# Kernel optimization log

Hardware: AMD Instinct MI355X
Metric: run time of the kernel (lower is better)

Reference implementation:

```python
import jax, jax.numpy as jnp
import numpy as np

D_IN = 30


def setup_inputs() -> dict:
    key = jax.random.key(0)
    ks = jax.random.split(key, 12)
    N, E = 100000, 3200000
    h = jax.random.normal(ks[0], (N, D_IN), dtype=jnp.float32)
    edge_index = jax.random.randint(ks[1], (2, E), 0, N, dtype=jnp.int64)
    edge_weight = jax.random.uniform(ks[2], (E,), dtype=jnp.float32)
    s = 1.0 / np.sqrt(D_IN)
    convW = jax.random.uniform(ks[3], (D_IN, D_IN), jnp.float32, -s, s)
    convb = jax.random.uniform(ks[4], (D_IN,), jnp.float32, -s, s)
    w1 = jax.random.uniform(ks[5], (30, 10), jnp.float32, -s, s)
    b1 = jax.random.uniform(ks[6], (10,), jnp.float32, -s, s)
    s2 = 1.0 / np.sqrt(10)
    w2 = jax.random.uniform(ks[7], (10, 10), jnp.float32, -s2, s2)
    b2 = jax.random.uniform(ks[8], (10,), jnp.float32, -s2, s2)
    w3 = jax.random.uniform(ks[9], (10, 10), jnp.float32, -s2, s2)
    b3 = jax.random.uniform(ks[10], (10,), jnp.float32, -s2, s2)
    w4 = jax.random.uniform(ks[11], (10, 1), jnp.float32, -s2, s2)
    b4 = jnp.zeros((1,), jnp.float32)
    return {"h": h, "edge_index": edge_index, "edge_weight": edge_weight,
            "convW": convW, "convb": convb,
            "w1": w1, "b1": b1, "w2": w2, "b2": b2,
            "w3": w3, "b3": b3, "w4": w4, "b4": b4}


def gcn_conv(h, edge_index, edge_weight, W, b):
    N = h.shape[0]
    x = h @ W  # [N, 30] linear transform first (PyG GCNConv)
    loop = jnp.arange(N, dtype=edge_index.dtype)
    row = jnp.concatenate([edge_index[0], loop])  # sources
    col = jnp.concatenate([edge_index[1], loop])  # targets
    ew = jnp.concatenate([edge_weight, jnp.ones((N,), edge_weight.dtype)])
    deg = jax.ops.segment_sum(ew, col, num_segments=N)
    dis = jnp.where(deg > 0, jax.lax.rsqrt(deg), 0.0)
    norm = dis[row] * ew * dis[col]  # symmetric normalization
    msg = x[row] * norm[:, None]  # [E+N, 30] gather + scale
    out = jax.ops.segment_sum(msg, col, num_segments=N)  # scatter-add
    return out + b


def reference(h, edge_index, edge_weight, convW, convb,
              w1, b1, w2, b2, w3, b3, w4, b4):
    x = jax.nn.relu(gcn_conv(h, edge_index, edge_weight, convW, convb))
    x = jax.nn.relu(x @ w1 + b1)
    x = jax.nn.relu(x @ w2 + b2)
    x = jax.nn.relu(x @ w3 + b3)
    x = jax.nn.sigmoid(x @ w4 + b4)
    return x[:, 0]
```

## Files before the change

kernel.cpp:

```cpp
#include <hip/hip_runtime.h>
#include <hip/hip_fp16.h>
#include <math.h>

#define D 30
#define FIXS 16777216.0f
#define FIXA 1048576.0f
#define BKT 128
#define LGB 7
#define CHUNK 8192
#define CAP 4608
#define ROWBITS 18
#define ROWMASK ((1u << ROWBITS) - 1)
#define MAXBKT 1024

__global__ __launch_bounds__(1024) void scatter1p_kernel(const int* __restrict__ row,
                                                         const int* __restrict__ col,
                                                         const float* __restrict__ ew,
                                                         unsigned* __restrict__ ecnt,
                                                         uint2* __restrict__ keysw,
                                                         int E, int nbkt) {
    __shared__ unsigned gcur[MAXBKT];
    __shared__ unsigned lofs[MAXBKT];
    __shared__ unsigned lcnt[MAXBKT];
    __shared__ unsigned sscan[1024];
    __shared__ uint2 st[CHUNK];
    __shared__ unsigned short bkt[CHUNK];
    const int t = threadIdx.x;
    for (int i = t; i < nbkt; i += 1024) lcnt[i] = 0;
    __syncthreads();

    const int e0 = blockIdx.x * CHUNK;
    const int e1 = min(e0 + CHUNK, E);
    const int cc = e1 - e0;
    const int nv = cc >> 2;
    const int4* c4 = (const int4*)(col + e0);

    for (int i = t; i < nv; i += 1024) {
        const int4 c = c4[i];
        atomicAdd(&lcnt[c.x >> LGB], 1u);
        atomicAdd(&lcnt[c.y >> LGB], 1u);
        atomicAdd(&lcnt[c.z >> LGB], 1u);
        atomicAdd(&lcnt[c.w >> LGB], 1u);
    }
    for (int e = e0 + (nv << 2) + t; e < e1; e += 1024) atomicAdd(&lcnt[col[e] >> LGB], 1u);
    __syncthreads();

    {
        const unsigned v = (t < nbkt) ? lcnt[t] : 0u;
        sscan[t] = v;
        for (int off = 1; off < 1024; off <<= 1) {
            __syncthreads();
            const unsigned x = (t >= off) ? sscan[t - off] : 0u;
            __syncthreads();
            sscan[t] += x;
        }
        __syncthreads();
        if (t < nbkt) {
            lofs[t] = sscan[t] - v;
            gcur[t] = (v > 0) ? atomicAdd(&ecnt[t], v) : 0u;
            lcnt[t] = 0;
        }
    }
    __syncthreads();

    const int4* r4 = (const int4*)(row + e0);
    const float4* w4 = (const float4*)(ew + e0);
    for (int i = t; i < nv; i += 1024) {
        const int4 c = c4[i];
        const int4 r = r4[i];
        const float4 w = w4[i];
#define PLACE(cx, rx, wx)                                                            \
        {                                                                            \
            const int b_ = (cx) >> LGB;                                              \
            const unsigned p_ = lofs[b_] + atomicAdd(&lcnt[b_], 1u);                 \
            st[p_] = make_uint2(((unsigned)((cx) & (BKT - 1)) << ROWBITS) |          \
                                (unsigned)(rx), __float_as_uint(wx));                \
            bkt[p_] = (unsigned short)b_;                                            \
        }
        PLACE(c.x, r.x, w.x)
        PLACE(c.y, r.y, w.y)
        PLACE(c.z, r.z, w.z)
        PLACE(c.w, r.w, w.w)
    }
    for (int e = e0 + (nv << 2) + t; e < e1; e += 1024) {
        const int cx = col[e];
        const int b_ = cx >> LGB;
        const unsigned p_ = lofs[b_] + atomicAdd(&lcnt[b_], 1u);
        st[p_] = make_uint2(((unsigned)(cx & (BKT - 1)) << ROWBITS) | (unsigned)row[e],
                            __float_as_uint(ew[e]));
        bkt[p_] = (unsigned short)b_;
    }
    __syncthreads();

    for (int p = t; p < cc; p += 1024) {
        const int b_ = bkt[p];
        const unsigned off = gcur[b_] + ((unsigned)p - lofs[b_]);
        if (off < CAP)
            keysw[(size_t)b_ * CAP + off] = st[p];
    }
}

__global__ __launch_bounds__(512) void degdis_kernel(const unsigned* __restrict__ ecnt,
                                                     const uint2* __restrict__ keysw,
                                                     float* __restrict__ dis, int N) {
    __shared__ unsigned degf[BKT];
    const int t = threadIdx.x;
    if (t < BKT) degf[t] = 0;
    __syncthreads();
    const int b = blockIdx.x;
    const uint2* kbase = keysw + (size_t)b * CAP;
    const unsigned ne = min(ecnt[b], (unsigned)CAP);
    for (unsigned e = t; e < ne; e += 512) {
        const uint2 kw = kbase[e];
        atomicAdd(&degf[kw.x >> ROWBITS], (unsigned)(__uint_as_float(kw.y) * FIXS));
    }
    __syncthreads();
    const int n = b * BKT + t;
    if (t < BKT && n < N)
        dis[n] = rsqrtf((float)degf[t] * (1.0f / FIXS) + 1.0f);
}

__global__ __launch_bounds__(256) void gemm_kernel(const float* __restrict__ h,
                                                   const float* __restrict__ W,
                                                   const float* __restrict__ dis,
                                                   uint4* __restrict__ yp4, int N) {
    __shared__ float hs[256 * D];
    __shared__ float Ws[D * D];
    const int t = threadIdx.x;
    const int nb = blockIdx.x * 256;
    const int cnt = min(256, N - nb);
    const int total = cnt * D;

    for (int i = t; i < D * D; i += 256) Ws[i] = W[i];
    for (int i = t; i < total; i += 256) hs[i] = h[nb * D + i];
    __syncthreads();

    float x[D];
    float dv = 0.f;
    if (t < cnt) {
#pragma unroll
        for (int j = 0; j < D; ++j) x[j] = 0.f;
#pragma unroll
        for (int k = 0; k < D; ++k) {
            const float hv = hs[t * D + k];
#pragma unroll
            for (int j = 0; j < D; ++j) x[j] += hv * Ws[k * D + j];
        }
        dv = dis[nb + t];
    }
    __syncthreads();
    __half* hsh = (__half*)hs;
    if (t < cnt) {
#pragma unroll
        for (int j = 0; j < D; ++j) hsh[t * 32 + j] = __float2half_rn(x[j] * dv);
        hsh[t * 32 + 30] = __float2half_rn(0.f);
        hsh[t * 32 + 31] = __float2half_rn(0.f);
    }
    __syncthreads();
    const uint4* hv4 = (const uint4*)hs;
    for (int i = t; i < cnt * 4; i += 256) yp4[nb * 4 + i] = hv4[i];
}

__global__ __launch_bounds__(512) void aggmlp_kernel(const uint4* __restrict__ yp4,
                                                     const float* __restrict__ dis,
                                                     const unsigned* __restrict__ ecnt,
                                                     const uint2* __restrict__ keysw,
                                                     const float* __restrict__ convb,
                                                     const float* __restrict__ w1,
                                                     const float* __restrict__ b1,
                                                     const float* __restrict__ w2,
                                                     const float* __restrict__ b2,
                                                     const float* __restrict__ w3,
                                                     const float* __restrict__ b3,
                                                     const float* __restrict__ w4,
                                                     const float* __restrict__ b4,
                                                     float* __restrict__ out, int N) {
    __shared__ int acci[BKT * 32];
    __shared__ float cb[D];
    __shared__ float W1[300], B1[10], W2[100], B2[10], W3[100], B3[10], W4[10], B4v[1];
    const int t = threadIdx.x;
    if (t < D) cb[t] = convb[t];
    if (t < 300) W1[t] = w1[t];
    if (t < 100) W2[t] = w2[t];
    if (t >= 128 && t < 228) W3[t - 128] = w3[t - 128];
    if (t < 10) { B1[t] = b1[t]; B2[t] = b2[t]; B3[t] = b3[t]; W4[t] = w4[t]; }
    if (t == 0) B4v[0] = b4[0];

    const int b = blockIdx.x;
    const int nb = b * BKT;
    const int cnt = min(BKT, N - nb);

    for (int i = t; i < cnt * 4; i += 512) {
        const int n = i >> 2, qq = i & 3;
        const uint4 v = yp4[(size_t)(nb + n) * 4 + qq];
        const __half2* hh = (const __half2*)&v;
        const float2 f0 = __half22float2(hh[0]);
        const float2 f1 = __half22float2(hh[1]);
        const float2 f2 = __half22float2(hh[2]);
        const float2 f3 = __half22float2(hh[3]);
        const int bo = n << 5, sw = n & 31, wb = qq << 3;
        acci[bo + ((wb + 0) ^ sw)] = __float2int_rn(f0.x * FIXA);
        acci[bo + ((wb + 1) ^ sw)] = __float2int_rn(f0.y * FIXA);
        acci[bo + ((wb + 2) ^ sw)] = __float2int_rn(f1.x * FIXA);
        acci[bo + ((wb + 3) ^ sw)] = __float2int_rn(f1.y * FIXA);
        acci[bo + ((wb + 4) ^ sw)] = __float2int_rn(f2.x * FIXA);
        acci[bo + ((wb + 5) ^ sw)] = __float2int_rn(f2.y * FIXA);
        acci[bo + ((wb + 6) ^ sw)] = __float2int_rn(f3.x * FIXA);
        acci[bo + ((wb + 7) ^ sw)] = __float2int_rn(f3.y * FIXA);
    }
    __syncthreads();

    const uint2* kbase = keysw + (size_t)b * CAP;
    const int ne = (int)min(ecnt[b], (unsigned)CAP);
    const int m = ne * 4;

#define EDGE(kw, q)                                                                  \
    {                                                                                \
        const float wf = __uint_as_float((kw).y) * FIXA;                             \
        const uint4 v = yp4[(size_t)((kw).x & ROWMASK) * 4 + (q)];                   \
        const __half2* hh = (const __half2*)&v;                                      \
        const float2 f0 = __half22float2(hh[0]);                                     \
        const float2 f1 = __half22float2(hh[1]);                                     \
        const float2 f2 = __half22float2(hh[2]);                                     \
        const float2 f3 = __half22float2(hh[3]);                                     \
        const int loc = (int)((kw).x >> ROWBITS);                                    \
        const int bo = loc << 5;                                                     \
        const int sw = loc & 31;                                                     \
        const int wb = (q) << 3;                                                     \
        atomicAdd(&acci[bo + ((wb + 0) ^ sw)], __float2int_rn(f0.x * wf));           \
        atomicAdd(&acci[bo + ((wb + 1) ^ sw)], __float2int_rn(f0.y * wf));           \
        atomicAdd(&acci[bo + ((wb + 2) ^ sw)], __float2int_rn(f1.x * wf));           \
        atomicAdd(&acci[bo + ((wb + 3) ^ sw)], __float2int_rn(f1.y * wf));           \
        atomicAdd(&acci[bo + ((wb + 4) ^ sw)], __float2int_rn(f2.x * wf));           \
        atomicAdd(&acci[bo + ((wb + 5) ^ sw)], __float2int_rn(f2.y * wf));           \
        atomicAdd(&acci[bo + ((wb + 6) ^ sw)], __float2int_rn(f3.x * wf));           \
        atomicAdd(&acci[bo + ((wb + 7) ^ sw)], __float2int_rn(f3.y * wf));           \
    }

    for (int i = t; i < m; i += 1024) {
        const int iB = i + 512;
        const uint2 kwA = kbase[i >> 2];
        const int qA = i & 3;
        if (iB < m) {
            const uint2 kwB = kbase[iB >> 2];
            const int qB = iB & 3;
            EDGE(kwA, qA)
            EDGE(kwB, qB)
        } else {
            EDGE(kwA, qA)
        }
    }
    __syncthreads();

    if (t < cnt) {
        const int nn = nb + t;
        const float dv = dis[nn] * (1.0f / FIXA);
        const int bo = t << 5;
        const int sw = t & 31;
        float v[D];
#pragma unroll
        for (int j = 0; j < D; ++j)
            v[j] = fmaxf(dv * (float)acci[bo + (j ^ sw)] + cb[j], 0.f);
        float h1[10];
#pragma unroll
        for (int j = 0; j < 10; ++j) h1[j] = B1[j];
#pragma unroll
        for (int k = 0; k < D; ++k) {
            const float vv = v[k];
#pragma unroll
            for (int j = 0; j < 10; ++j) h1[j] += vv * W1[k * 10 + j];
        }
#pragma unroll
        for (int j = 0; j < 10; ++j) h1[j] = fmaxf(h1[j], 0.f);
        float h2[10];
#pragma unroll
        for (int j = 0; j < 10; ++j) h2[j] = B2[j];
#pragma unroll
        for (int k = 0; k < 10; ++k) {
            const float vv = h1[k];
#pragma unroll
            for (int j = 0; j < 10; ++j) h2[j] += vv * W2[k * 10 + j];
        }
#pragma unroll
        for (int j = 0; j < 10; ++j) h2[j] = fmaxf(h2[j], 0.f);
        float h3[10];
#pragma unroll
        for (int j = 0; j < 10; ++j) h3[j] = B3[j];
#pragma unroll
        for (int k = 0; k < 10; ++k) {
            const float vv = h2[k];
#pragma unroll
            for (int j = 0; j < 10; ++j) h3[j] += vv * W3[k * 10 + j];
        }
#pragma unroll
        for (int j = 0; j < 10; ++j) h3[j] = fmaxf(h3[j], 0.f);
        float z = B4v[0];
#pragma unroll
        for (int k = 0; k < 10; ++k) z += h3[k] * W4[k];
        out[nn] = 1.f / (1.f + expf(-z));
    }
}

extern "C" void kernel_launch(void* const* d_in, const int* in_sizes, int n_in,
                              void* d_out, int out_size, void* d_ws, size_t ws_size,
                              hipStream_t stream) {
    const float* h   = (const float*)d_in[0];
    const int*   ei  = (const int*)d_in[1];
    const float* ew  = (const float*)d_in[2];
    const float* convW = (const float*)d_in[3];
    const float* convb = (const float*)d_in[4];
    const float* w1 = (const float*)d_in[5];
    const float* b1 = (const float*)d_in[6];
    const float* w2 = (const float*)d_in[7];
    const float* b2 = (const float*)d_in[8];
    const float* w3 = (const float*)d_in[9];
    const float* b3 = (const float*)d_in[10];
    const float* w4 = (const float*)d_in[11];
    const float* b4 = (const float*)d_in[12];
    float* out = (float*)d_out;

    const int N = in_sizes[0] / D;
    const int E = in_sizes[2];
    const int* row = ei;
    const int* col = ei + E;

    const int nbkt = (N + BKT - 1) >> LGB;
    const int nchunks = (E + CHUNK - 1) / CHUNK;
    const int nblk256 = (N + 255) / 256;

    __half* yp = (__half*)d_ws;
    uint2* keysw = (uint2*)(yp + (size_t)N * 32);
    float* dis = (float*)(keysw + (size_t)nbkt * CAP);
    unsigned* ecnt = (unsigned*)(dis + N);

    hipMemsetAsync(ecnt, 0, (size_t)nbkt * sizeof(unsigned), stream);

    scatter1p_kernel<<<nchunks, 1024, 0, stream>>>(row, col, ew, ecnt, keysw, E, nbkt);
    degdis_kernel<<<nbkt, 512, 0, stream>>>(ecnt, keysw, dis, N);
    gemm_kernel<<<nblk256, 256, 0, stream>>>(h, convW, dis, (uint4*)yp, N);
    aggmlp_kernel<<<nbkt, 512, 0, stream>>>((const uint4*)yp, dis, ecnt, keysw, convb,
                                            w1, b1, w2, b2, w3, b3, w4, b4, out, N);
}
```

Before: 94.45 us.

## Load edge keys once per lane, shuffle across quads, batch four gathers

The scatter loop now has each thread load one edge key, then share keys across groups of four lanes with warp shuffles. Each lane issues four independent row gathers up front before doing its atomics, which should raise memory-level parallelism and remove the redundant key loads of the old one-key-per-four-lanes pattern. The GEMM tile load of h also switches to float4 vector loads. The risk is more registers, per-edge bounds predicates, and reliance on the nb*D offset staying 16-byte aligned.

```diff
diff --git a/kernel.cpp b/kernel.cpp
--- a/kernel.cpp
+++ b/kernel.cpp
@@ -132,7 +132,13 @@
     const int total = cnt * D;
 
     for (int i = t; i < D * D; i += 256) Ws[i] = W[i];
-    for (int i = t; i < total; i += 256) hs[i] = h[nb * D + i];
+    {
+        const float4* h4 = (const float4*)(h + (size_t)nb * D);
+        float4* hs4 = (float4*)hs;
+        const int nf4 = total >> 2;
+        for (int i = t; i < nf4; i += 256) hs4[i] = h4[i];
+        for (int i = (nf4 << 2) + t; i < total; i += 256) hs[i] = h[(size_t)nb * D + i];
+    }
     __syncthreads();
 
     float x[D];
@@ -212,21 +218,21 @@
 
     const uint2* kbase = keysw + (size_t)b * CAP;
     const int ne = (int)min(ecnt[b], (unsigned)CAP);
-    const int m = ne * 4;
-
-#define EDGE(kw, q)                                                                  \
+    const int q = t & 3;
+    const int eg0 = (t >> 2) << 2;
+
+#define EDGE2(kx, ky, v)                                                             \
     {                                                                                \
-        const float wf = __uint_as_float((kw).y) * FIXA;                             \
-        const uint4 v = yp4[(size_t)((kw).x & ROWMASK) * 4 + (q)];                   \
-        const __half2* hh = (const __half2*)&v;                                      \
+        const float wf = __uint_as_float(ky) * FIXA;                                 \
+        const __half2* hh = (const __half2*)&(v);                                    \
         const float2 f0 = __half22float2(hh[0]);                                     \
         const float2 f1 = __half22float2(hh[1]);                                     \
         const float2 f2 = __half22float2(hh[2]);                                     \
         const float2 f3 = __half22float2(hh[3]);                                     \
-        const int loc = (int)((kw).x >> ROWBITS);                                    \
+        const int loc = (int)((kx) >> ROWBITS);                                      \
         const int bo = loc << 5;                                                     \
         const int sw = loc & 31;                                                     \
-        const int wb = (q) << 3;                                                     \
+        const int wb = q << 3;                                                       \
         atomicAdd(&acci[bo + ((wb + 0) ^ sw)], __float2int_rn(f0.x * wf));           \
         atomicAdd(&acci[bo + ((wb + 1) ^ sw)], __float2int_rn(f0.y * wf));           \
         atomicAdd(&acci[bo + ((wb + 2) ^ sw)], __float2int_rn(f1.x * wf));           \
@@ -237,18 +243,30 @@
         atomicAdd(&acci[bo + ((wb + 7) ^ sw)], __float2int_rn(f3.y * wf));           \
     }
 
-    for (int i = t; i < m; i += 1024) {
-        const int iB = i + 512;
-        const uint2 kwA = kbase[i >> 2];
-        const int qA = i & 3;
-        if (iB < m) {
-            const uint2 kwB = kbase[iB >> 2];
-            const int qB = iB & 3;
-            EDGE(kwA, qA)
-            EDGE(kwB, qB)
-        } else {
-            EDGE(kwA, qA)
-        }
+    for (int base = 0; base < ne; base += 512) {
+        const int myE = base + t;
+        uint2 km = make_uint2(0u, 0u);
+        if (myE < ne) km = kbase[myE];
+        const unsigned long long kull =
+            ((unsigned long long)km.y << 32) | (unsigned long long)km.x;
+        const int l0 = t & ~3;
+        const unsigned long long ks0 = __shfl(kull, l0 + 0);
+        const unsigned long long ks1 = __shfl(kull, l0 + 1);
+        const unsigned long long ks2 = __shfl(kull, l0 + 2);
+        const unsigned long long ks3 = __shfl(kull, l0 + 3);
+        const unsigned kx0 = (unsigned)ks0, ky0 = (unsigned)(ks0 >> 32);
+        const unsigned kx1 = (unsigned)ks1, ky1 = (unsigned)(ks1 >> 32);
+        const unsigned kx2 = (unsigned)ks2, ky2 = (unsigned)(ks2 >> 32);
+        const unsigned kx3 = (unsigned)ks3, ky3 = (unsigned)(ks3 >> 32);
+        const uint4 v0 = yp4[(size_t)(kx0 & ROWMASK) * 4 + q];
+        const uint4 v1 = yp4[(size_t)(kx1 & ROWMASK) * 4 + q];
+        const uint4 v2 = yp4[(size_t)(kx2 & ROWMASK) * 4 + q];
+        const uint4 v3 = yp4[(size_t)(kx3 & ROWMASK) * 4 + q];
+        const int eg = base + eg0;
+        if (eg + 0 < ne) EDGE2(kx0, ky0, v0)
+        if (eg + 1 < ne) EDGE2(kx1, ky1, v1)
+        if (eg + 2 < ne) EDGE2(kx2, ky2, v2)
+        if (eg + 3 < ne) EDGE2(kx3, ky3, v3)
     }
     __syncthreads();
 
```

After: 98.53 us. 1.04x slower.
